# Kernel optimization log

Measured on AMD Instinct MI355X. Metric: run time of the kernel, lower is better.

Reference implementation:

```python
import jax, jax.numpy as jnp
import numpy as np

D_MODEL = 1024
NUM_HEADS = 16
HEAD_DIM = D_MODEL // NUM_HEADS  # 64
# NOTE: the original module passes scale=attention_head_size, so scores are
# MULTIPLIED by head_dim (64), not divided by sqrt(head_dim). Faithful quirk.
SCALE = float(HEAD_DIM)


def setup_inputs() -> dict:
    key = jax.random.key(0)
    ks = jax.random.split(key, 6)
    bs, s, d = 2, 2048, D_MODEL
    q = jax.random.normal(ks[0], (bs, s, d), dtype=jnp.float32)
    k = jax.random.normal(ks[1], (bs, s, d), dtype=jnp.float32)
    v = jax.random.normal(ks[2], (bs, s, d), dtype=jnp.float32)
    # nn.Linear weights, shape (out, in); no bias (qkv_bias=False)
    init = 1.0 / np.sqrt(d)
    Wq = jax.random.uniform(ks[3], (d, d), jnp.float32, -init, init)
    Wk = jax.random.uniform(ks[4], (d, d), jnp.float32, -init, init)
    Wv = jax.random.uniform(ks[5], (d, d), jnp.float32, -init, init)
    return {"q": q, "k": k, "v": v, "Wq": Wq, "Wk": Wk, "Wv": Wv}


def _split_heads(x):
    bs, s, _ = x.shape
    return x.reshape(bs, s, NUM_HEADS, HEAD_DIM).transpose(0, 2, 1, 3)  # bhsd


def reference(q, k, v, Wq, Wk, Wv):
    bs, s, d = q.shape
    qh = _split_heads(q @ Wq.T)  # [b,h,s,hd]
    kh = _split_heads(k @ Wk.T)
    vh = _split_heads(v @ Wv.T)
    sims = jnp.einsum('bhqd,bhkd->bhqk', qh, kh) * SCALE
    attn = jax.nn.softmax(sims, axis=-1)
    out = jnp.einsum('bhqk,bhkd->bhqd', attn, vh)  # [b,h,s,hd]
    out = out.transpose(0, 2, 1, 3).reshape(bs, s, d)
    return out
```

## Files before the change

kernel.cpp:

```cpp
#include <hip/hip_runtime.h>


typedef _Float16 half4 __attribute__((ext_vector_type(4)));
typedef _Float16 half8 __attribute__((ext_vector_type(8)));
typedef float floatx4 __attribute__((ext_vector_type(4)));

#define MFMA_F16(a, b, c) __builtin_amdgcn_mfma_f32_16x16x32_f16((a), (b), (c), 0, 0, 0)

constexpr int SEQ = 2048;
constexpr int DM = 1024;
constexpr int NH = 16;
constexpr int HD = 64;
constexpr float QSCALE = 92.33248261689366f;

__device__ __forceinline__ void gl2lds16(const _Float16* g, _Float16* l) {
  __builtin_amdgcn_global_load_lds(
      (const __attribute__((address_space(1))) void*)g,
      (__attribute__((address_space(3))) void*)l, 16, 0, 0);
}

__device__ inline void split4(const float4 f, half4& h, half4& l) {
  h[0] = (_Float16)f.x; l[0] = (_Float16)(f.x - (float)h[0]);
  h[1] = (_Float16)f.y; l[1] = (_Float16)(f.y - (float)h[1]);
  h[2] = (_Float16)f.z; l[2] = (_Float16)(f.z - (float)h[2]);
  h[3] = (_Float16)f.w; l[3] = (_Float16)(f.w - (float)h[3]);
}

__global__ __launch_bounds__(256) void convert_kernel(
    const float* __restrict__ x, const float* __restrict__ W,
    _Float16* __restrict__ xh, _Float16* __restrict__ xl,
    _Float16* __restrict__ Wh, _Float16* __restrict__ Wl, int do_lo)
{
  if (blockIdx.x < 4096) {
    int idx = blockIdx.x * 256 + threadIdx.x;
    float4 f = ((const float4*)x)[idx];
    half4 h, l; split4(f, h, l);
    *(half4*)(xh + (size_t)idx * 4) = h;
    if (do_lo) *(half4*)(xl + (size_t)idx * 4) = l;
  } else {
    int idx = (blockIdx.x - 4096) * 256 + threadIdx.x;
    float4 f = ((const float4*)W)[idx];
    half4 h, l; split4(f, h, l);
    *(half4*)(Wh + (size_t)idx * 4) = h;
    if (do_lo) *(half4*)(Wl + (size_t)idx * 4) = l;
  }
}

__global__ __launch_bounds__(256, 1) void proj_kernel(
    const _Float16* __restrict__ Ahg, const _Float16* __restrict__ Alg,
    const _Float16* __restrict__ Bhg, const _Float16* __restrict__ Blg,
    _Float16* __restrict__ yh, _Float16* __restrict__ yl,
    float scale, int three)
{
  __shared__ __align__(16) _Float16 Ahs[2][128][64];
  __shared__ __align__(16) _Float16 Als[2][128][64];
  __shared__ __align__(16) _Float16 Bhs[2][128][64];
  __shared__ __align__(16) _Float16 Bls[2][128][64];

  const int tid = threadIdx.x;
  const int bm = blockIdx.x;
  const int bn = blockIdx.y;
  const int lane = tid & 63, l15 = lane & 15, quad = lane >> 4;
  const int w = tid >> 6, wm = w >> 1, wn = w & 1;

  const int r8 = lane >> 3;
  const int cp8 = (((lane & 7) ^ r8)) * 8;
  int grow[4];
  #pragma unroll
  for (int i = 0; i < 4; i++) grow[i] = (w * 4 + i) * 8 + r8;

  floatx4 acc[4][4];
  #pragma unroll
  for (int mt = 0; mt < 4; mt++)
    #pragma unroll
    for (int nt = 0; nt < 4; nt++)
      acc[mt][nt] = (floatx4){0.f, 0.f, 0.f, 0.f};

  #pragma unroll
  for (int i = 0; i < 4; i++) {
    const int g = w * 4 + i;
    const size_t ga = (size_t)(bm * 128 + grow[i]) * DM + cp8;
    const size_t gb = (size_t)(bn * 128 + grow[i]) * DM + cp8;
    gl2lds16(Ahg + ga, &Ahs[0][0][0] + g * 512);
    gl2lds16(Bhg + gb, &Bhs[0][0][0] + g * 512);
    if (three) {
      gl2lds16(Alg + ga, &Als[0][0][0] + g * 512);
      gl2lds16(Blg + gb, &Bls[0][0][0] + g * 512);
    }
  }

  for (int t = 0; t < 16; t++) {
    const int cur = t & 1;
    __syncthreads();
    if (t + 1 < 16) {
      const int kk = (t + 1) * 64, nxt = cur ^ 1;
      #pragma unroll
      for (int i = 0; i < 4; i++) {
        const int g = w * 4 + i;
        const size_t ga = (size_t)(bm * 128 + grow[i]) * DM + kk + cp8;
        const size_t gb = (size_t)(bn * 128 + grow[i]) * DM + kk + cp8;
        gl2lds16(Ahg + ga, &Ahs[nxt][0][0] + g * 512);
        gl2lds16(Bhg + gb, &Bhs[nxt][0][0] + g * 512);
        if (three) {
          gl2lds16(Alg + ga, &Als[nxt][0][0] + g * 512);
          gl2lds16(Blg + gb, &Bls[nxt][0][0] + g * 512);
        }
      }
    }

    #pragma unroll
    for (int kc = 0; kc < 2; kc++) {
      const int swz = ((kc * 4 + quad) ^ (l15 & 7)) * 8;
      half8 ah[4], bh_[4], al[4], bl[4];
      #pragma unroll
      for (int tt = 0; tt < 4; tt++) {
        ah[tt]  = *(const half8*)&Ahs[cur][wm * 64 + tt * 16 + l15][swz];
        bh_[tt] = *(const half8*)&Bhs[cur][wn * 64 + tt * 16 + l15][swz];
        if (three) {
          al[tt] = *(const half8*)&Als[cur][wm * 64 + tt * 16 + l15][swz];
          bl[tt] = *(const half8*)&Bls[cur][wn * 64 + tt * 16 + l15][swz];
        }
      }
      if (three) {
        #pragma unroll
        for (int mt = 0; mt < 4; mt++)
          #pragma unroll
          for (int nt = 0; nt < 4; nt++) {
            floatx4 t0 = MFMA_F16(ah[mt], bh_[nt], acc[mt][nt]);
            t0 = MFMA_F16(ah[mt], bl[nt], t0);
            acc[mt][nt] = MFMA_F16(al[mt], bh_[nt], t0);
          }
      } else {
        #pragma unroll
        for (int mt = 0; mt < 4; mt++)
          #pragma unroll
          for (int nt = 0; nt < 4; nt++)
            acc[mt][nt] = MFMA_F16(ah[mt], bh_[nt], acc[mt][nt]);
      }
    }
  }

  #pragma unroll
  for (int mt = 0; mt < 4; mt++)
    #pragma unroll
    for (int nt = 0; nt < 4; nt++)
      #pragma unroll
      for (int r = 0; r < 4; r++) {
        int gm = bm * 128 + wm * 64 + mt * 16 + quad * 4 + r;
        int gn = bn * 128 + wn * 64 + nt * 16 + l15;
        int b = gm >> 11, s = gm & 2047;
        int h = gn >> 6, d = gn & 63;
        size_t idx = ((size_t)(b * NH + h) * SEQ + s) * HD + d;
        float val = acc[mt][nt][r] * scale;
        _Float16 hi = (_Float16)val;
        yh[idx] = hi;
        if (three) yl[idx] = (_Float16)(val - (float)hi);
      }
}

__global__ __launch_bounds__(256) void transpose_v(const _Float16* __restrict__ vh,
                                                   _Float16* __restrict__ vhT)
{
  __shared__ __align__(16) _Float16 T[128][72];
  const int bh = blockIdx.x, sc = blockIdx.y, tid = threadIdx.x;
  const _Float16* src = vh + ((size_t)bh * SEQ + sc * 128) * HD;
  #pragma unroll
  for (int i = 0; i < 4; i++) {
    int c = i * 256 + tid, row = c >> 3, off = (c & 7) * 8;
    *(half8*)&T[row][off] = *(const half8*)(src + (size_t)row * HD + off);
  }
  __syncthreads();
  _Float16* dst = vhT + (size_t)bh * HD * SEQ + sc * 128;
  #pragma unroll
  for (int i = 0; i < 4; i++) {
    int c = i * 256 + tid, hd = c >> 4, off = (c & 15) * 8;
    int base32 = off & ~31, qsel = (off >> 3) & 3;
    half8 vv;
    #pragma unroll
    for (int j = 0; j < 8; j++) {
      int s_local = base32 + 16 * (j >> 2) + 4 * qsel + (j & 3);
      vv[j] = T[s_local][hd];
    }
    *(half8*)(dst + (size_t)hd * SEQ + off) = vv;
  }
}

__global__ __launch_bounds__(256, 4) void flash_kernel(
    const _Float16* __restrict__ qh_hi, const _Float16* __restrict__ qh_lo,
    const _Float16* __restrict__ kh_hi, const _Float16* __restrict__ kh_lo,
    const _Float16* __restrict__ vhT, float* __restrict__ Op, float2* __restrict__ ml)
{
  __shared__ __align__(16) _Float16 Kh[2][64][64];
  __shared__ __align__(16) _Float16 Kl[2][64][64];
  __shared__ __align__(16) _Float16 Vt[64][64];

  const int id = blockIdx.x;
  const int seq_ = id >> 3;
  const int bh = (id & 7) + 8 * (seq_ & 3);
  const int rem = seq_ >> 2;
  const int qb = rem & 15;
  const int kh = rem >> 4;
  const int tid = threadIdx.x;
  const int wq = tid >> 6;
  const int lane = tid & 63, l15 = lane & 15, quad = lane >> 4;

  const size_t bh_off = (size_t)bh * SEQ * HD;
  const _Float16* __restrict__ kh_p = kh_hi + bh_off;
  const _Float16* __restrict__ kl_p = kh_lo + bh_off;
  const _Float16* __restrict__ vt_p = vhT + (size_t)bh * HD * SEQ;
  const int qrow0 = qb * 128 + wq * 32;

  half8 bqh[2][2], bql[2][2];
  #pragma unroll
  for (int g = 0; g < 2; g++) {
    const _Float16* qp_h = qh_hi + bh_off + (size_t)(qrow0 + g * 16 + l15) * HD;
    const _Float16* qp_l = qh_lo + bh_off + (size_t)(qrow0 + g * 16 + l15) * HD;
    #pragma unroll
    for (int kc = 0; kc < 2; kc++) {
      bqh[g][kc] = *(const half8*)(qp_h + kc * 32 + quad * 8);
      bql[g][kc] = *(const half8*)(qp_l + kc * 32 + quad * 8);
    }
  }

  const int r8 = lane >> 3;
  const int cp8 = ((lane & 7) ^ r8) * 8;

  float m_[2] = {-3.0e38f, -3.0e38f};
  float l_[2] = {0.f, 0.f};
  floatx4 Oacc[2][4];
  #pragma unroll
  for (int g = 0; g < 2; g++)
    #pragma unroll
    for (int nd = 0; nd < 4; nd++) Oacc[g][nd] = (floatx4){0.f, 0.f, 0.f, 0.f};

  const int kt0 = kh * 16;
  {
    const int kbase = kt0 * 64;
    #pragma unroll
    for (int i = 0; i < 2; i++) {
      const int g = wq * 2 + i;
      const int r = g * 8 + r8;
      gl2lds16(kh_p + (size_t)(kbase + r) * HD + cp8, &Kh[0][0][0] + g * 512);
      gl2lds16(kl_p + (size_t)(kbase + r) * HD + cp8, &Kl[0][0][0] + g * 512);
    }
  }

  for (int kt = kt0; kt < kt0 + 16; kt++) {
    const int cur = kt & 1;
    const int kbase = kt * 64;
    __syncthreads();

    #pragma unroll
    for (int i = 0; i < 2; i++) {
      const int g = wq * 2 + i;
      const int r = g * 8 + r8;
      gl2lds16(vt_p + (size_t)r * SEQ + kbase + cp8, &Vt[0][0] + g * 512);
    }
    if (kt + 1 < kt0 + 16) {
      const int kb2 = (kt + 1) * 64, nxt = cur ^ 1;
      #pragma unroll
      for (int i = 0; i < 2; i++) {
        const int g = wq * 2 + i;
        const int r = g * 8 + r8;
        gl2lds16(kh_p + (size_t)(kb2 + r) * HD + cp8, &Kh[nxt][0][0] + g * 512);
        gl2lds16(kl_p + (size_t)(kb2 + r) * HD + cp8, &Kl[nxt][0][0] + g * 512);
      }
    }

    floatx4 sacc[2][4];
    const int r7 = l15 & 7;
    #pragma unroll
    for (int nt = 0; nt < 4; nt++) {
      half8 akh0 = *(const half8*)&Kh[cur][nt * 16 + l15][((0 * 4 + quad) ^ r7) * 8];
      half8 akh1 = *(const half8*)&Kh[cur][nt * 16 + l15][((1 * 4 + quad) ^ r7) * 8];
      half8 akl0 = *(const half8*)&Kl[cur][nt * 16 + l15][((0 * 4 + quad) ^ r7) * 8];
      half8 akl1 = *(const half8*)&Kl[cur][nt * 16 + l15][((1 * 4 + quad) ^ r7) * 8];
      #pragma unroll
      for (int g = 0; g < 2; g++) {
        floatx4 s4 = (floatx4){0.f, 0.f, 0.f, 0.f};
        s4 = MFMA_F16(akh0, bqh[g][0], s4);
        s4 = MFMA_F16(akh1, bqh[g][1], s4);
        s4 = MFMA_F16(akh0, bql[g][0], s4);
        s4 = MFMA_F16(akh1, bql[g][1], s4);
        s4 = MFMA_F16(akl0, bqh[g][0], s4);
        s4 = MFMA_F16(akl1, bqh[g][1], s4);
        sacc[g][nt] = s4;
      }
    }

    float alpha2[2];
    half8 bp8g[2][2];
    #pragma unroll
    for (int g = 0; g < 2; g++) {
      float rmax = sacc[g][0][0];
      #pragma unroll
      for (int nt = 0; nt < 4; nt++)
        #pragma unroll
        for (int r = 0; r < 4; r++) rmax = fmaxf(rmax, sacc[g][nt][r]);
      rmax = fmaxf(rmax, __shfl_xor(rmax, 16, 64));
      rmax = fmaxf(rmax, __shfl_xor(rmax, 32, 64));
      const float mnew = fmaxf(m_[g], rmax);
      alpha2[g] = exp2f(m_[g] - mnew);
      m_[g] = mnew;

      float rsum = 0.f;
      #pragma unroll
      for (int nt = 0; nt < 4; nt++)
        #pragma unroll
        for (int r = 0; r < 4; r++) {
          float p = exp2f(sacc[g][nt][r] - mnew);
          sacc[g][nt][r] = p;
          rsum += p;
        }
      rsum += __shfl_xor(rsum, 16, 64);
      rsum += __shfl_xor(rsum, 32, 64);
      l_[g] = l_[g] * alpha2[g] + rsum;

      #pragma unroll
      for (int kc = 0; kc < 2; kc++)
        #pragma unroll
        for (int j = 0; j < 8; j++)
          bp8g[g][kc][j] = (_Float16)sacc[g][2 * kc + (j >> 2)][j & 3];
    }

    __syncthreads();

    half8 av[4][2];
    #pragma unroll
    for (int nd = 0; nd < 4; nd++) {
      av[nd][0] = *(const half8*)&Vt[nd * 16 + l15][((0 * 4 + quad) ^ r7) * 8];
      av[nd][1] = *(const half8*)&Vt[nd * 16 + l15][((1 * 4 + quad) ^ r7) * 8];
    }

    #pragma unroll
    for (int g = 0; g < 2; g++) {
      #pragma unroll
      for (int nd = 0; nd < 4; nd++) {
        Oacc[g][nd][0] *= alpha2[g]; Oacc[g][nd][1] *= alpha2[g];
        Oacc[g][nd][2] *= alpha2[g]; Oacc[g][nd][3] *= alpha2[g];
        Oacc[g][nd] = MFMA_F16(av[nd][0], bp8g[g][0], Oacc[g][nd]);
        Oacc[g][nd] = MFMA_F16(av[nd][1], bp8g[g][1], Oacc[g][nd]);
      }
    }
  }

  const size_t fqbase = (size_t)bh * SEQ + qrow0;
  #pragma unroll
  for (int g = 0; g < 2; g++) {
    const size_t fq = fqbase + g * 16 + l15;
    float* ob = Op + ((size_t)kh * 65536 + fq) * HD;
    #pragma unroll
    for (int nd = 0; nd < 4; nd++) {
      float4 vv;
      vv.x = Oacc[g][nd][0]; vv.y = Oacc[g][nd][1];
      vv.z = Oacc[g][nd][2]; vv.w = Oacc[g][nd][3];
      *(float4*)(ob + nd * 16 + quad * 4) = vv;
    }
    if (quad == 0) ml[kh * 65536 + fq] = make_float2(m_[g], l_[g]);
  }
}

__global__ __launch_bounds__(256) void merge_kernel(const float* __restrict__ Op,
                                                    const float2* __restrict__ ml,
                                                    float* __restrict__ out)
{
  const int tid = threadIdx.x;
  const int fq = blockIdx.x * 64 + (tid >> 2);
  const int dp = (tid & 3) * 16;
  float2 m0 = ml[fq], m1 = ml[65536 + fq];
  float M = fmaxf(m0.x, m1.x);
  float w0 = exp2f(m0.x - M), w1 = exp2f(m1.x - M);
  float rinv = 1.0f / (m0.y * w0 + m1.y * w1);
  int bh = fq >> 11, s = fq & 2047, b = bh >> 4, h = bh & 15;
  float* ob = out + ((size_t)(b * SEQ + s)) * DM + h * HD + dp;
  const float* p0 = Op + (size_t)fq * HD + dp;
  const float* p1 = p0 + (size_t)65536 * HD;
  #pragma unroll
  for (int j = 0; j < 4; j++) {
    float4 a = *(const float4*)(p0 + 4 * j);
    float4 c = *(const float4*)(p1 + 4 * j);
    float4 r;
    r.x = (a.x * w0 + c.x * w1) * rinv;
    r.y = (a.y * w0 + c.y * w1) * rinv;
    r.z = (a.z * w0 + c.z * w1) * rinv;
    r.w = (a.w * w0 + c.w * w1) * rinv;
    *(float4*)(ob + 4 * j) = r;
  }
}

extern "C" void kernel_launch(void* const* d_in, const int* in_sizes, int n_in,
                              void* d_out, int out_size, void* d_ws, size_t ws_size,
                              hipStream_t stream) {
  const float* q  = (const float*)d_in[0];
  const float* k  = (const float*)d_in[1];
  const float* v  = (const float*)d_in[2];
  const float* Wq = (const float*)d_in[3];
  const float* Wk = (const float*)d_in[4];
  const float* Wv = (const float*)d_in[5];
  float* out = (float*)d_out;

  char* W = (char*)d_ws;
  const size_t MiB = 1ull << 20;
  _Float16* qh_hi = (_Float16*)(W + 0 * MiB);
  _Float16* qh_lo = (_Float16*)(W + 8 * MiB);
  _Float16* kh_hi = (_Float16*)(W + 16 * MiB);
  _Float16* kh_lo = (_Float16*)(W + 24 * MiB);
  _Float16* vhT   = (_Float16*)(W + 32 * MiB);
  _Float16* vh    = (_Float16*)(W + 40 * MiB);
  _Float16* xh    = (_Float16*)(W + 48 * MiB);
  _Float16* xl    = (_Float16*)(W + 56 * MiB);
  _Float16* Wh    = (_Float16*)(W + 64 * MiB);
  _Float16* Wl    = (_Float16*)(W + 66 * MiB);
  float*    Op    = (float*)  (W + 40 * MiB);
  float2*   mlp   = (float2*) (W + 72 * MiB);

  convert_kernel<<<5120, 256, 0, stream>>>(q, Wq, xh, xl, Wh, Wl, 1);
  proj_kernel<<<dim3(32, 8), 256, 0, stream>>>(xh, xl, Wh, Wl, qh_hi, qh_lo, QSCALE, 1);
  convert_kernel<<<5120, 256, 0, stream>>>(k, Wk, xh, xl, Wh, Wl, 1);
  proj_kernel<<<dim3(32, 8), 256, 0, stream>>>(xh, xl, Wh, Wl, kh_hi, kh_lo, 1.0f, 1);
  convert_kernel<<<5120, 256, 0, stream>>>(v, Wv, xh, xl, Wh, Wl, 0);
  proj_kernel<<<dim3(32, 8), 256, 0, stream>>>(xh, xl, Wh, Wl, vh, vh, 1.0f, 0);

  transpose_v<<<dim3(32, 16), 256, 0, stream>>>(vh, vhT);
  flash_kernel<<<1024, 256, 0, stream>>>(qh_hi, qh_lo, kh_hi, kh_lo, vhT, Op, mlp);
  merge_kernel<<<1024, 256, 0, stream>>>(Op, mlp, out);
}
```

Before: 322.0 us.

## Batch Q/K/V conversion and projection into single launches; add MFMA priority hints

Merges the three convert launches into one kernel and the three projection GEMMs into one launch with a z-dimension over Q/K/V, so 768 blocks run concurrently instead of three serialized waves of 256. The projection drops LDS double buffering in favour of a single buffer synchronised before and after each load, which halves LDS use but exposes load latency. s_setprio hints are also added around the MFMA sections of the flash kernel. Workspace grows to hold separate converted buffers for each input.

```diff
diff --git a/kernel.cpp b/kernel.cpp
--- a/kernel.cpp
+++ b/kernel.cpp
@@ -26,36 +26,58 @@
   h[3] = (_Float16)f.w; l[3] = (_Float16)(f.w - (float)h[3]);
 }
 
-__global__ __launch_bounds__(256) void convert_kernel(
-    const float* __restrict__ x, const float* __restrict__ W,
-    _Float16* __restrict__ xh, _Float16* __restrict__ xl,
-    _Float16* __restrict__ Wh, _Float16* __restrict__ Wl, int do_lo)
+__global__ __launch_bounds__(256) void convert_all(
+    const float* __restrict__ q, const float* __restrict__ k,
+    const float* __restrict__ v, const float* __restrict__ Wq,
+    const float* __restrict__ Wk, const float* __restrict__ Wv,
+    _Float16* __restrict__ xq_h, _Float16* __restrict__ xq_l,
+    _Float16* __restrict__ xk_h, _Float16* __restrict__ xk_l,
+    _Float16* __restrict__ xv_h,
+    _Float16* __restrict__ Wqh, _Float16* __restrict__ Wql,
+    _Float16* __restrict__ Wkh, _Float16* __restrict__ Wkl,
+    _Float16* __restrict__ Wvh)
 {
-  if (blockIdx.x < 4096) {
-    int idx = blockIdx.x * 256 + threadIdx.x;
-    float4 f = ((const float4*)x)[idx];
-    half4 h, l; split4(f, h, l);
-    *(half4*)(xh + (size_t)idx * 4) = h;
-    if (do_lo) *(half4*)(xl + (size_t)idx * 4) = l;
-  } else {
-    int idx = (blockIdx.x - 4096) * 256 + threadIdx.x;
-    float4 f = ((const float4*)W)[idx];
-    half4 h, l; split4(f, h, l);
-    *(half4*)(Wh + (size_t)idx * 4) = h;
-    if (do_lo) *(half4*)(Wl + (size_t)idx * 4) = l;
-  }
-}
-
-__global__ __launch_bounds__(256, 1) void proj_kernel(
-    const _Float16* __restrict__ Ahg, const _Float16* __restrict__ Alg,
-    const _Float16* __restrict__ Bhg, const _Float16* __restrict__ Blg,
-    _Float16* __restrict__ yh, _Float16* __restrict__ yl,
-    float scale, int three)
+  const int bid = blockIdx.x;
+  const float* src; _Float16* dh; _Float16* dl; int do_lo, i0;
+  if (bid < 4096)       { src = q;  dh = xq_h; dl = xq_l; do_lo = 1; i0 = bid; }
+  else if (bid < 8192)  { src = k;  dh = xk_h; dl = xk_l; do_lo = 1; i0 = bid - 4096; }
+  else if (bid < 12288) { src = v;  dh = xv_h; dl = xv_h; do_lo = 0; i0 = bid - 8192; }
+  else if (bid < 13312) { src = Wq; dh = Wqh;  dl = Wql;  do_lo = 1; i0 = bid - 12288; }
+  else if (bid < 14336) { src = Wk; dh = Wkh;  dl = Wkl;  do_lo = 1; i0 = bid - 13312; }
+  else                  { src = Wv; dh = Wvh;  dl = Wvh;  do_lo = 0; i0 = bid - 14336; }
+  const int idx = i0 * 256 + threadIdx.x;
+  float4 f = ((const float4*)src)[idx];
+  half4 h, l; split4(f, h, l);
+  *(half4*)(dh + (size_t)idx * 4) = h;
+  if (do_lo) *(half4*)(dl + (size_t)idx * 4) = l;
+}
+
+__global__ __launch_bounds__(256, 1) void proj3_kernel(
+    const _Float16* __restrict__ xq_h, const _Float16* __restrict__ xq_l,
+    const _Float16* __restrict__ xk_h, const _Float16* __restrict__ xk_l,
+    const _Float16* __restrict__ xv_h,
+    const _Float16* __restrict__ Wqh, const _Float16* __restrict__ Wql,
+    const _Float16* __restrict__ Wkh, const _Float16* __restrict__ Wkl,
+    const _Float16* __restrict__ Wvh,
+    _Float16* __restrict__ qh_hi, _Float16* __restrict__ qh_lo,
+    _Float16* __restrict__ kh_hi, _Float16* __restrict__ kh_lo,
+    _Float16* __restrict__ vh)
 {
-  __shared__ __align__(16) _Float16 Ahs[2][128][64];
-  __shared__ __align__(16) _Float16 Als[2][128][64];
-  __shared__ __align__(16) _Float16 Bhs[2][128][64];
-  __shared__ __align__(16) _Float16 Bls[2][128][64];
+  __shared__ __align__(16) _Float16 Ahs[128][64];
+  __shared__ __align__(16) _Float16 Als[128][64];
+  __shared__ __align__(16) _Float16 Bhs[128][64];
+  __shared__ __align__(16) _Float16 Bls[128][64];
+
+  const int z = blockIdx.z;
+  const _Float16 *Ahg, *Alg, *Bhg, *Blg;
+  _Float16 *yh, *yl;
+  float scale; int three;
+  if (z == 0)      { Ahg = xq_h; Alg = xq_l; Bhg = Wqh; Blg = Wql;
+                     yh = qh_hi; yl = qh_lo; scale = QSCALE; three = 1; }
+  else if (z == 1) { Ahg = xk_h; Alg = xk_l; Bhg = Wkh; Blg = Wkl;
+                     yh = kh_hi; yl = kh_lo; scale = 1.0f; three = 1; }
+  else             { Ahg = xv_h; Alg = xv_h; Bhg = Wvh; Blg = Wvh;
+                     yh = vh;    yl = vh;    scale = 1.0f; three = 0; }
 
   const int tid = threadIdx.x;
   const int bm = blockIdx.x;
@@ -65,9 +87,16 @@
 
   const int r8 = lane >> 3;
   const int cp8 = (((lane & 7) ^ r8)) * 8;
-  int grow[4];
-  #pragma unroll
-  for (int i = 0; i < 4; i++) grow[i] = (w * 4 + i) * 8 + r8;
+  int grow[4]; _Float16* la[4]; _Float16* lal[4]; _Float16* lb[4]; _Float16* lbl[4];
+  #pragma unroll
+  for (int i = 0; i < 4; i++) {
+    const int g = w * 4 + i;
+    grow[i] = g * 8 + r8;
+    la[i]  = &Ahs[0][0] + g * 512;
+    lal[i] = &Als[0][0] + g * 512;
+    lb[i]  = &Bhs[0][0] + g * 512;
+    lbl[i] = &Bls[0][0] + g * 512;
+  }
 
   floatx4 acc[4][4];
   #pragma unroll
@@ -76,49 +105,32 @@
     for (int nt = 0; nt < 4; nt++)
       acc[mt][nt] = (floatx4){0.f, 0.f, 0.f, 0.f};
 
-  #pragma unroll
-  for (int i = 0; i < 4; i++) {
-    const int g = w * 4 + i;
-    const size_t ga = (size_t)(bm * 128 + grow[i]) * DM + cp8;
-    const size_t gb = (size_t)(bn * 128 + grow[i]) * DM + cp8;
-    gl2lds16(Ahg + ga, &Ahs[0][0][0] + g * 512);
-    gl2lds16(Bhg + gb, &Bhs[0][0][0] + g * 512);
-    if (three) {
-      gl2lds16(Alg + ga, &Als[0][0][0] + g * 512);
-      gl2lds16(Blg + gb, &Bls[0][0][0] + g * 512);
-    }
-  }
-
-  for (int t = 0; t < 16; t++) {
-    const int cur = t & 1;
+  for (int kk = 0; kk < DM; kk += 64) {
     __syncthreads();
-    if (t + 1 < 16) {
-      const int kk = (t + 1) * 64, nxt = cur ^ 1;
-      #pragma unroll
-      for (int i = 0; i < 4; i++) {
-        const int g = w * 4 + i;
-        const size_t ga = (size_t)(bm * 128 + grow[i]) * DM + kk + cp8;
-        const size_t gb = (size_t)(bn * 128 + grow[i]) * DM + kk + cp8;
-        gl2lds16(Ahg + ga, &Ahs[nxt][0][0] + g * 512);
-        gl2lds16(Bhg + gb, &Bhs[nxt][0][0] + g * 512);
-        if (three) {
-          gl2lds16(Alg + ga, &Als[nxt][0][0] + g * 512);
-          gl2lds16(Blg + gb, &Bls[nxt][0][0] + g * 512);
-        }
-      }
-    }
+    #pragma unroll
+    for (int i = 0; i < 4; i++) {
+      const size_t ga = (size_t)(bm * 128 + grow[i]) * DM + kk + cp8;
+      const size_t gb = (size_t)(bn * 128 + grow[i]) * DM + kk + cp8;
+      gl2lds16(Ahg + ga, la[i]);
+      gl2lds16(Bhg + gb, lb[i]);
+      if (three) {
+        gl2lds16(Alg + ga, lal[i]);
+        gl2lds16(Blg + gb, lbl[i]);
+      }
+    }
+    __syncthreads();
 
     #pragma unroll
     for (int kc = 0; kc < 2; kc++) {
       const int swz = ((kc * 4 + quad) ^ (l15 & 7)) * 8;
       half8 ah[4], bh_[4], al[4], bl[4];
       #pragma unroll
-      for (int tt = 0; tt < 4; tt++) {
-        ah[tt]  = *(const half8*)&Ahs[cur][wm * 64 + tt * 16 + l15][swz];
-        bh_[tt] = *(const half8*)&Bhs[cur][wn * 64 + tt * 16 + l15][swz];
+      for (int t = 0; t < 4; t++) {
+        ah[t]  = *(const half8*)&Ahs[wm * 64 + t * 16 + l15][swz];
+        bh_[t] = *(const half8*)&Bhs[wn * 64 + t * 16 + l15][swz];
         if (three) {
-          al[tt] = *(const half8*)&Als[cur][wm * 64 + tt * 16 + l15][swz];
-          bl[tt] = *(const half8*)&Bls[cur][wn * 64 + tt * 16 + l15][swz];
+          al[t] = *(const half8*)&Als[wm * 64 + t * 16 + l15][swz];
+          bl[t] = *(const half8*)&Bls[wn * 64 + t * 16 + l15][swz];
         }
       }
       if (three) {
@@ -269,6 +281,7 @@
 
     floatx4 sacc[2][4];
     const int r7 = l15 & 7;
+    __builtin_amdgcn_s_setprio(1);
     #pragma unroll
     for (int nt = 0; nt < 4; nt++) {
       half8 akh0 = *(const half8*)&Kh[cur][nt * 16 + l15][((0 * 4 + quad) ^ r7) * 8];
@@ -287,6 +300,7 @@
         sacc[g][nt] = s4;
       }
     }
+    __builtin_amdgcn_s_setprio(0);
 
     float alpha2[2];
     half8 bp8g[2][2];
@@ -332,6 +346,7 @@
       av[nd][1] = *(const half8*)&Vt[nd * 16 + l15][((1 * 4 + quad) ^ r7) * 8];
     }
 
+    __builtin_amdgcn_s_setprio(1);
     #pragma unroll
     for (int g = 0; g < 2; g++) {
       #pragma unroll
@@ -342,6 +357,7 @@
         Oacc[g][nd] = MFMA_F16(av[nd][1], bp8g[g][1], Oacc[g][nd]);
       }
     }
+    __builtin_amdgcn_s_setprio(0);
   }
 
   const size_t fqbase = (size_t)bh * SEQ + qrow0;
@@ -407,20 +423,25 @@
   _Float16* kh_lo = (_Float16*)(W + 24 * MiB);
   _Float16* vhT   = (_Float16*)(W + 32 * MiB);
   _Float16* vh    = (_Float16*)(W + 40 * MiB);
-  _Float16* xh    = (_Float16*)(W + 48 * MiB);
-  _Float16* xl    = (_Float16*)(W + 56 * MiB);
-  _Float16* Wh    = (_Float16*)(W + 64 * MiB);
-  _Float16* Wl    = (_Float16*)(W + 66 * MiB);
+  _Float16* xq_h  = (_Float16*)(W + 48 * MiB);
+  _Float16* xq_l  = (_Float16*)(W + 56 * MiB);
+  _Float16* xk_h  = (_Float16*)(W + 64 * MiB);
+  _Float16* xk_l  = (_Float16*)(W + 72 * MiB);
+  _Float16* xv_h  = (_Float16*)(W + 80 * MiB);
+  _Float16* Wqh   = (_Float16*)(W + 88 * MiB);
+  _Float16* Wql   = (_Float16*)(W + 90 * MiB);
+  _Float16* Wkh   = (_Float16*)(W + 92 * MiB);
+  _Float16* Wkl   = (_Float16*)(W + 94 * MiB);
+  _Float16* Wvh   = (_Float16*)(W + 96 * MiB);
   float*    Op    = (float*)  (W + 40 * MiB);
-  float2*   mlp   = (float2*) (W + 72 * MiB);
-
-  convert_kernel<<<5120, 256, 0, stream>>>(q, Wq, xh, xl, Wh, Wl, 1);
-  proj_kernel<<<dim3(32, 8), 256, 0, stream>>>(xh, xl, Wh, Wl, qh_hi, qh_lo, QSCALE, 1);
-  convert_kernel<<<5120, 256, 0, stream>>>(k, Wk, xh, xl, Wh, Wl, 1);
-  proj_kernel<<<dim3(32, 8), 256, 0, stream>>>(xh, xl, Wh, Wl, kh_hi, kh_lo, 1.0f, 1);
-  convert_kernel<<<5120, 256, 0, stream>>>(v, Wv, xh, xl, Wh, Wl, 0);
-  proj_kernel<<<dim3(32, 8), 256, 0, stream>>>(xh, xl, Wh, Wl, vh, vh, 1.0f, 0);
-
+  float2*   mlp   = (float2*) (W + 98 * MiB);
+
+  convert_all<<<15360, 256, 0, stream>>>(q, k, v, Wq, Wk, Wv,
+                                         xq_h, xq_l, xk_h, xk_l, xv_h,
+                                         Wqh, Wql, Wkh, Wkl, Wvh);
+  proj3_kernel<<<dim3(32, 8, 3), 256, 0, stream>>>(
+      xq_h, xq_l, xk_h, xk_l, xv_h, Wqh, Wql, Wkh, Wkl, Wvh,
+      qh_hi, qh_lo, kh_hi, kh_lo, vh);
   transpose_v<<<dim3(32, 16), 256, 0, stream>>>(vh, vhT);
   flash_kernel<<<1024, 256, 0, stream>>>(qh_hi, qh_lo, kh_hi, kh_lo, vhT, Op, mlp);
   merge_kernel<<<1024, 256, 0, stream>>>(Op, mlp, out);
```

Result: faster. 295.4 us (-8.3%).
